# Kernel tuning notes

Hardware: AMD Instinct MI355X
Metric: run time of the kernel (lower is better)

## Reference

```python
import jax, jax.numpy as jnp
import numpy as np
import math

E_LENGTH = 64


def setup_inputs() -> dict:
    key = jax.random.key(0)
    ks = jax.random.split(key, 9)
    B, L, D, N, H = 4, 1024, 1024, 16, 64
    scale = 0.05  # emulate xavier-normal scale
    return {
        "x": jax.random.normal(ks[0], (B, L, D), dtype=jnp.float32),
        "mask": jnp.ones((B, L), dtype=jnp.int32),
        "w_q": jax.random.normal(ks[1], (N, D, H), dtype=jnp.float32) * scale,
        "w_k": jax.random.normal(ks[2], (N, D, H), dtype=jnp.float32) * scale,
        "w_v": jax.random.normal(ks[3], (N, D, H), dtype=jnp.float32) * scale,
        "w_o": jax.random.normal(ks[4], (N, H, D), dtype=jnp.float32) * scale,
        "q_embed_table": jax.random.normal(ks[5], (2 * E_LENGTH - 1, H), dtype=jnp.float32) * scale,
        "k_embed_table": jax.random.normal(ks[6], (2 * E_LENGTH - 1, H), dtype=jnp.float32) * scale,
        "v_embed_table": jax.random.normal(ks[7], (2 * E_LENGTH - 1, H), dtype=jnp.float32) * scale,
    }


def reference(x, mask, w_q, w_k, w_v, w_o, q_embed_table, k_embed_table, v_embed_table):
    # x: [B, L, d_model], mask: [B, L]
    L = x.shape[1]
    d_qkv = w_q.shape[-1]
    e = E_LENGTH

    q = jnp.einsum('blm,nmh->bnlh', x, w_q)
    k = jnp.einsum('blm,nmh->bnlh', x, w_k)
    v = jnp.einsum('blm,nmh->bnlh', x, w_v)

    pos = jnp.arange(L)
    # clipped relative distance indices in [0, 2e-2]
    dist = jnp.clip(pos[:, None] - pos[None, :], -(e - 1), e - 1) + (e - 1)  # [L, L]

    scores = jnp.einsum('bnid,bnjd->bnij', q, k)
    # mode contains 'q': key-side bias uses k_embedding
    k_embed = k_embed_table[dist]  # [L, L, d]
    scores = scores + jnp.einsum('bnjd,ijd->bnij', k, k_embed)
    # mode contains 'k': query-side bias uses q_embedding
    q_embed = q_embed_table[dist]  # [L, L, d]
    scores = scores + jnp.einsum('bnid,ijd->bnij', q, q_embed)

    scores = scores / math.sqrt(d_qkv)
    scores = jnp.where((mask == 0)[:, None, None, :], jnp.float32(-1e9), scores)
    p_attn = jax.nn.softmax(scores, axis=-1)  # [B, N, L, L]

    out = jnp.einsum('bnij,bnjd->bnid', p_attn, v)
    # mode contains 'v': value-side relative bias
    v_embed = v_embed_table[dist]  # [L, L, d]
    out = out + jnp.einsum('bnij,ijd->bnid', p_attn, v_embed)

    # per-head output projection, then sum over heads
    return jnp.einsum('bnid,ndm->bim', out, w_o)
```

## Files before the change

kernel.cpp:

```cpp
#include <hip/hip_runtime.h>


typedef __bf16 bf16x8 __attribute__((ext_vector_type(8)));
typedef float f32x4 __attribute__((ext_vector_type(4)));
typedef unsigned int u32x4 __attribute__((ext_vector_type(4)));
typedef unsigned short u16x4 __attribute__((ext_vector_type(4)));

__device__ __forceinline__ unsigned short f2bf(float f) {
    unsigned int u = __builtin_bit_cast(unsigned int, f);
    u += 0x7fffu + ((u >> 16) & 1u);
    return (unsigned short)(u >> 16);
}
__device__ __forceinline__ float bf2f(unsigned short s) {
    unsigned int u = ((unsigned int)s) << 16;
    return __builtin_bit_cast(float, u);
}

__device__ __forceinline__ void gl2lds16(const unsigned short* g, unsigned short* l) {
    __builtin_amdgcn_global_load_lds(
        (const __attribute__((address_space(1))) unsigned int*)g,
        (__attribute__((address_space(3))) unsigned int*)l, 16, 0, 0);
}

__global__ __launch_bounds__(256) void convert_kernel(
    const float* __restrict__ x,
    const float* __restrict__ wq,
    const float* __restrict__ wk,
    const float* __restrict__ wv,
    const float* __restrict__ wo,
    const float* __restrict__ qe,
    const float* __restrict__ ke,
    const float* __restrict__ ve,
    unsigned short* __restrict__ x_bf,
    unsigned short* __restrict__ wqkv_bt,
    unsigned short* __restrict__ wo_bt,
    unsigned short* __restrict__ qe_bf,
    unsigned short* __restrict__ ke_bf,
    unsigned short* __restrict__ ve_t)
{
    __shared__ unsigned short T[64 * 72];
    const int bid = blockIdx.x;
    const int tid = threadIdx.x;

    if (bid < 512) {
        const float* src = x + (size_t)bid * 8192;
        unsigned short* dst = x_bf + (size_t)bid * 8192;
#pragma unroll
        for (int c = 0; c < 8; ++c) {
            int idx = c * 1024 + tid * 4;
            f32x4 v = *reinterpret_cast<const f32x4*>(src + idx);
            u16x4 o = u16x4{f2bf(v[0]), f2bf(v[1]), f2bf(v[2]), f2bf(v[3])};
            *reinterpret_cast<u16x4*>(dst + idx) = o;
        }
    } else if (bid < 1280) {
        int t = bid - 512;
        int which = t >> 8, n = (t >> 4) & 15, dt = t & 15;
        const float* w = which == 0 ? wq : which == 1 ? wk : wv;
        const float* src = w + ((size_t)n * 1024 + dt * 64) * 64;
#pragma unroll
        for (int c = 0; c < 4; ++c) {
            int chunk = c * 256 + tid;
            int dd = chunk >> 4, hh = (chunk & 15) * 4;
            f32x4 v = *reinterpret_cast<const f32x4*>(src + dd * 64 + hh);
#pragma unroll
            for (int j = 0; j < 4; ++j) T[(hh + j) * 72 + dd] = f2bf(v[j]);
        }
        __syncthreads();
        unsigned short* dstb = wqkv_bt + ((size_t)(which * 1024 + n * 64)) * 1024 + dt * 64;
#pragma unroll
        for (int c = 0; c < 2; ++c) {
            int chunk = c * 256 + tid;
            int h = chunk >> 3, d8 = (chunk & 7) * 8;
            u32x4 v = *reinterpret_cast<const u32x4*>(&T[h * 72 + d8]);
            *reinterpret_cast<u32x4*>(dstb + (size_t)h * 1024 + d8) = v;
        }
    } else if (bid < 1536) {
        int t = bid - 1280;
        int n = t >> 4, mt = t & 15;
        const float* src = wo + (size_t)n * 64 * 1024 + mt * 64;
#pragma unroll
        for (int c = 0; c < 4; ++c) {
            int chunk = c * 256 + tid;
            int hh = chunk >> 4, mm = (chunk & 15) * 4;
            f32x4 v = *reinterpret_cast<const f32x4*>(src + (size_t)hh * 1024 + mm);
#pragma unroll
            for (int j = 0; j < 4; ++j) T[(mm + j) * 72 + hh] = f2bf(v[j]);
        }
        __syncthreads();
        unsigned short* dstb = wo_bt + (size_t)(mt * 64) * 1024 + n * 64;
#pragma unroll
        for (int c = 0; c < 2; ++c) {
            int chunk = c * 256 + tid;
            int m = chunk >> 3, h8 = (chunk & 7) * 8;
            u32x4 v = *reinterpret_cast<const u32x4*>(&T[m * 72 + h8]);
            *reinterpret_cast<u32x4*>(dstb + (size_t)m * 1024 + h8) = v;
        }
    } else {
        for (int i = tid; i < 8192; i += 256) {
            int e = i >> 6;
            qe_bf[i] = (e < 127) ? f2bf(qe[i]) : 0;
            ke_bf[i] = (e < 127) ? f2bf(ke[i]) : 0;
            int h = i >> 7, e2 = i & 127;
            ve_t[i] = (e2 < 127) ? f2bf(ve[e2 * 64 + h]) : 0;
        }
    }
}

__global__ __launch_bounds__(256) void gemm_qkv_kernel(
    const unsigned short* __restrict__ A,
    const unsigned short* __restrict__ Bt,
    unsigned short* __restrict__ q_buf,
    unsigned short* __restrict__ k_buf,
    unsigned short* __restrict__ v_t)
{
    __shared__ unsigned short Sh[2 * 128 * 64];
    unsigned short* As = Sh;
    unsigned short* Bs = Sh + 8192;
    const int m0 = blockIdx.y * 128;
    const int n0 = blockIdx.x * 128;
    const int tid = threadIdx.x;
    const int lane = tid & 63;
    const int w = tid >> 6;
    const int wr = w >> 1, wc = w & 1;
    const int g = lane >> 4, c16 = lane & 15;

    f32x4 acc[4][4];
#pragma unroll
    for (int i = 0; i < 4; ++i)
#pragma unroll
        for (int j = 0; j < 4; ++j) acc[i][j] = f32x4{0.f, 0.f, 0.f, 0.f};

    for (int kt = 0; kt < 1024; kt += 64) {
#pragma unroll
        for (int c = 0; c < 4; ++c) {
            int chunk = c * 256 + tid;
            int row = chunk >> 3, col = (chunk & 7) * 8;
            unsigned short* ldsA = &As[(c * 256 + w * 64) * 8];
            unsigned short* ldsB = &Bs[(c * 256 + w * 64) * 8];
            gl2lds16(A  + (size_t)(m0 + row) * 1024 + kt + col, ldsA);
            gl2lds16(Bt + (size_t)(n0 + row) * 1024 + kt + col, ldsB);
        }
        __syncthreads();
#pragma unroll
        for (int ks = 0; ks < 2; ++ks) {
            bf16x8 af[4], bfr[4];
#pragma unroll
            for (int mi = 0; mi < 4; ++mi)
                af[mi] = __builtin_bit_cast(bf16x8,
                    *reinterpret_cast<const u32x4*>(&As[(wr * 64 + mi * 16 + c16) * 64 + ks * 32 + g * 8]));
#pragma unroll
            for (int ni = 0; ni < 4; ++ni)
                bfr[ni] = __builtin_bit_cast(bf16x8,
                    *reinterpret_cast<const u32x4*>(&Bs[(wc * 64 + ni * 16 + c16) * 64 + ks * 32 + g * 8]));
#pragma unroll
            for (int mi = 0; mi < 4; ++mi)
#pragma unroll
                for (int ni = 0; ni < 4; ++ni)
                    acc[mi][ni] = __builtin_amdgcn_mfma_f32_16x16x32_bf16(af[mi], bfr[ni], acc[mi][ni], 0, 0, 0);
        }
        __syncthreads();
    }

    if (n0 < 2048) {
#pragma unroll
        for (int mi = 0; mi < 4; ++mi)
#pragma unroll
            for (int ni = 0; ni < 4; ++ni)
#pragma unroll
                for (int r = 0; r < 4; ++r) {
                    int m = m0 + wr * 64 + mi * 16 + g * 4 + r;
                    int c = n0 + wc * 64 + ni * 16 + c16;
                    int b = m >> 10, l = m & 1023;
                    int which = c >> 10, n = (c >> 6) & 15, h = c & 63;
                    unsigned short* dst = which == 0 ? q_buf : k_buf;
                    dst[(((size_t)b * 16 + n) * 1024 + l) * 64 + h] = f2bf(acc[mi][ni][r]);
                }
    } else {
#pragma unroll
        for (int mi = 0; mi < 4; ++mi)
#pragma unroll
            for (int ni = 0; ni < 4; ++ni)
#pragma unroll
                for (int r = 0; r < 4; ++r) {
                    int l = wr * 64 + mi * 16 + g * 4 + r;
                    int cr = wc * 64 + ni * 16 + c16;
                    Sh[cr * 128 + (l ^ ((cr & 7) << 3))] = f2bf(acc[mi][ni][r]);
                }
        __syncthreads();
        const int b = m0 >> 10;
        const size_t rowbase = (size_t)(b * 1024 + (n0 - 2048)) * 1024 + (m0 & 1023);
#pragma unroll
        for (int c = 0; c < 8; ++c) {
            int chunk = c * 256 + tid;
            int cr = chunk >> 4, l0 = (chunk & 15) * 8;
            int lsw = l0 ^ ((cr & 7) << 3);
            u32x4 vv = *reinterpret_cast<const u32x4*>(&Sh[cr * 128 + lsw]);
            *reinterpret_cast<u32x4*>(v_t + rowbase + (size_t)cr * 1024 + l0) = vv;
        }
    }
}

__global__ __launch_bounds__(256) void proj_kernel(
    const unsigned short* __restrict__ q_buf,
    const unsigned short* __restrict__ k_buf,
    const unsigned short* __restrict__ qe_bf,
    const unsigned short* __restrict__ ke_bf,
    unsigned short* __restrict__ q_proj,
    unsigned short* __restrict__ k_proj,
    unsigned short* __restrict__ kp_edge)
{
    __shared__ unsigned short As[128 * 64];
    __shared__ unsigned short Bs[128 * 64];
    const int by = blockIdx.y;
    const int which = by >> 9;
    const int m0 = (by & 511) * 128;
    const unsigned short* A  = which ? k_buf : q_buf;
    const unsigned short* Bt = which ? ke_bf : qe_bf;
    unsigned short* C0 = which ? k_proj : q_proj;

    const int tid = threadIdx.x;
    const int lane = tid & 63;
    const int w = tid >> 6;
    const int wr = w >> 1, wc = w & 1;
    const int g = lane >> 4, c16 = lane & 15;

    f32x4 acc[4][4];
#pragma unroll
    for (int i = 0; i < 4; ++i)
#pragma unroll
        for (int j = 0; j < 4; ++j) acc[i][j] = f32x4{0.f, 0.f, 0.f, 0.f};

#pragma unroll
    for (int c = 0; c < 4; ++c) {
        int chunk = c * 256 + tid;
        int row = chunk >> 3, col = (chunk & 7) * 8;
        unsigned short* ldsA = &As[(c * 256 + w * 64) * 8];
        unsigned short* ldsB = &Bs[(c * 256 + w * 64) * 8];
        gl2lds16(A  + (size_t)(m0 + row) * 64 + col, ldsA);
        gl2lds16(Bt + (size_t)row * 64 + col, ldsB);
    }
    __syncthreads();
#pragma unroll
    for (int ks = 0; ks < 2; ++ks) {
        bf16x8 af[4], bfr[4];
#pragma unroll
        for (int mi = 0; mi < 4; ++mi)
            af[mi] = __builtin_bit_cast(bf16x8,
                *reinterpret_cast<const u32x4*>(&As[(wr * 64 + mi * 16 + c16) * 64 + ks * 32 + g * 8]));
#pragma unroll
        for (int ni = 0; ni < 4; ++ni)
            bfr[ni] = __builtin_bit_cast(bf16x8,
                *reinterpret_cast<const u32x4*>(&Bs[(wc * 64 + ni * 16 + c16) * 64 + ks * 32 + g * 8]));
#pragma unroll
        for (int mi = 0; mi < 4; ++mi)
#pragma unroll
            for (int ni = 0; ni < 4; ++ni)
                acc[mi][ni] = __builtin_amdgcn_mfma_f32_16x16x32_bf16(af[mi], bfr[ni], acc[mi][ni], 0, 0, 0);
    }

#pragma unroll
    for (int mi = 0; mi < 4; ++mi) {
#pragma unroll
        for (int ni = 0; ni < 4; ++ni) {
#pragma unroll
            for (int r = 0; r < 4; ++r) {
                int m = m0 + wr * 64 + mi * 16 + g * 4 + r;
                int c = wc * 64 + ni * 16 + c16;
                float v = acc[mi][ni][r];
                C0[(size_t)m * 128 + c] = f2bf(v);
                if (which && (c == 0 || c == 126))
                    kp_edge[(size_t)(c ? 65536 : 0) + m] = f2bf(v);
            }
        }
    }
}

__global__ __launch_bounds__(256) void gemm_n64_kernel(
    const unsigned short* __restrict__ A,
    const unsigned short* __restrict__ Bt,
    float* __restrict__ C)
{
    __shared__ unsigned short As[128 * 64];
    __shared__ unsigned short Bs[64 * 64];
    const int m0 = blockIdx.y * 128;
    const int n0 = blockIdx.x * 64;
    const int tid = threadIdx.x;
    const int lane = tid & 63;
    const int w = tid >> 6;
    const int g = lane >> 4, c16 = lane & 15;

    f32x4 acc[2][4];
#pragma unroll
    for (int i = 0; i < 2; ++i)
#pragma unroll
        for (int j = 0; j < 4; ++j) acc[i][j] = f32x4{0.f, 0.f, 0.f, 0.f};

    for (int kt = 0; kt < 1024; kt += 64) {
#pragma unroll
        for (int c = 0; c < 4; ++c) {
            int chunk = c * 256 + tid;
            int row = chunk >> 3, col = (chunk & 7) * 8;
            unsigned short* ldsA = &As[(c * 256 + w * 64) * 8];
            gl2lds16(A + (size_t)(m0 + row) * 1024 + kt + col, ldsA);
        }
#pragma unroll
        for (int c = 0; c < 2; ++c) {
            int chunk = c * 256 + tid;
            int row = chunk >> 3, col = (chunk & 7) * 8;
            unsigned short* ldsB = &Bs[(c * 256 + w * 64) * 8];
            gl2lds16(Bt + (size_t)(n0 + row) * 1024 + kt + col, ldsB);
        }
        __syncthreads();
#pragma unroll
        for (int ks = 0; ks < 2; ++ks) {
            bf16x8 af[2], bfr[4];
#pragma unroll
            for (int mi = 0; mi < 2; ++mi)
                af[mi] = __builtin_bit_cast(bf16x8,
                    *reinterpret_cast<const u32x4*>(&As[(w * 32 + mi * 16 + c16) * 64 + ks * 32 + g * 8]));
#pragma unroll
            for (int ni = 0; ni < 4; ++ni)
                bfr[ni] = __builtin_bit_cast(bf16x8,
                    *reinterpret_cast<const u32x4*>(&Bs[(ni * 16 + c16) * 64 + ks * 32 + g * 8]));
#pragma unroll
            for (int mi = 0; mi < 2; ++mi)
#pragma unroll
                for (int ni = 0; ni < 4; ++ni)
                    acc[mi][ni] = __builtin_amdgcn_mfma_f32_16x16x32_bf16(af[mi], bfr[ni], acc[mi][ni], 0, 0, 0);
        }
        __syncthreads();
    }

#pragma unroll
    for (int mi = 0; mi < 2; ++mi)
#pragma unroll
        for (int ni = 0; ni < 4; ++ni)
#pragma unroll
            for (int r = 0; r < 4; ++r) {
                int m = m0 + w * 32 + mi * 16 + g * 4 + r;
                int cc = n0 + ni * 16 + c16;
                C[(size_t)m * 1024 + cc] = acc[mi][ni][r];
            }
}

#define ATTN_LDS_BYTES 54784

__global__ __launch_bounds__(512, 4) void attn_kernel(
    const unsigned short* __restrict__ q_buf,
    const unsigned short* __restrict__ k_buf,
    const unsigned short* __restrict__ v_t,
    const unsigned short* __restrict__ q_proj,
    const unsigned short* __restrict__ k_proj,
    const unsigned short* __restrict__ kp_edge,
    const unsigned short* __restrict__ ve_t,
    const int* __restrict__ mask,
    unsigned short* __restrict__ attn_out)
{
    extern __shared__ char smem[];
    unsigned short* Ks = (unsigned short*)smem;
    unsigned short* Vt = (unsigned short*)(smem + 9216);
    unsigned short* Ps = (unsigned short*)(smem + 18432);
    unsigned short* kp = (unsigned short*)(smem + 36864);
    float* mj   = (float*)(smem + 54272);
    float* kpej = (float*)(smem + 54528);
    unsigned short* veT = (unsigned short*)smem;
    unsigned short* peB = (unsigned short*)(smem + 17408);
    float* lrow = (float*)(smem + 52224);

    const int id = blockIdx.x;
    const int bn = id & 63;
    const int ib = id >> 6;
    const int b = bn >> 4;
    const int i0 = ib * 128;
    const int tid = threadIdx.x;
    const int lane = tid & 63;
    const int w = tid >> 6;
    const int g = lane >> 4, c16 = lane & 15;
    const int il = tid >> 2;
    const int part = tid & 3;

    const int jlo = 2 * ib - 1, jhi = 2 * ib + 2;

    const int sr = tid >> 3,  sc = (tid & 7) * 8;

    bf16x8 qf[2];
    {
        const unsigned short* qrow = q_buf + ((size_t)bn * 1024 + i0 + w * 16 + c16) * 64;
        qf[0] = __builtin_bit_cast(bf16x8, *reinterpret_cast<const u32x4*>(qrow + g * 8));
        qf[1] = __builtin_bit_cast(bf16x8, *reinterpret_cast<const u32x4*>(qrow + 32 + g * 8));
    }
    f32x4 qp0v, qp126v;
#pragma unroll
    for (int r = 0; r < 4; ++r) {
        size_t row = (size_t)bn * 1024 + i0 + w * 16 + g * 4 + r;
        qp0v[r]   = 0.125f * bf2f(q_proj[row * 128 + 0]);
        qp126v[r] = 0.125f * bf2f(q_proj[row * 128 + 126]);
    }

    float peR[32];
#pragma unroll
    for (int k = 0; k < 32; ++k) peR[k] = 0.f;
    float lreg = 0.f, acc0 = 0.f, acc126 = 0.f;
    f32x4 accO[4];
#pragma unroll
    for (int i = 0; i < 4; ++i) accO[i] = f32x4{0.f, 0.f, 0.f, 0.f};

    for (int jt = 0; jt < 16; ++jt) {
        const int j0 = jt * 64;
        const bool need_kp = (jt >= jlo) && (jt <= jhi);

        {
            u32x4 kv = *reinterpret_cast<const u32x4*>(k_buf + ((size_t)bn * 1024 + j0 + sr) * 64 + sc);
            u32x4 vv = *reinterpret_cast<const u32x4*>(v_t + ((size_t)bn * 64 + sr) * 1024 + j0 + sc);
            *reinterpret_cast<u32x4*>(&Ks[sr * 72 + sc]) = kv;
            *reinterpret_cast<u32x4*>(&Vt[sr * 72 + sc]) = vv;
        }
        if (need_kp) {
#pragma unroll
            for (int c = 0; c < 2; ++c) {
                int chunk = tid + c * 512;
                int row = chunk >> 4, col = (chunk & 15) * 8;
                u32x4 v = *reinterpret_cast<const u32x4*>(k_proj + ((size_t)bn * 1024 + j0 + row) * 128 + col);
                *reinterpret_cast<u32x4*>(&kp[row * 136 + col]) = v;
            }
        }
        if (tid < 64) {
            mj[tid] = mask[b * 1024 + j0 + tid] ? 1.f : 0.f;
            kpej[tid] = 0.125f * bf2f(kp_edge[(size_t)(jt < 2 * ib ? 65536 : 0) + bn * 1024 + j0 + tid]);
        }
        __syncthreads();

        f32x4 sacc[4];
#pragma unroll
        for (int nf = 0; nf < 4; ++nf) sacc[nf] = f32x4{0.f, 0.f, 0.f, 0.f};
#pragma unroll
        for (int ks = 0; ks < 2; ++ks)
#pragma unroll
            for (int nf = 0; nf < 4; ++nf) {
                bf16x8 kf = __builtin_bit_cast(bf16x8,
                    *reinterpret_cast<const u32x4*>(&Ks[(nf * 16 + c16) * 72 + ks * 32 + g * 8]));
                sacc[nf] = __builtin_amdgcn_mfma_f32_16x16x32_bf16(qf[ks], kf, sacc[nf], 0, 0, 0);
            }

        const int dw = i0 + w * 16 - j0;
        if (dw < 126 && dw > -78) {
            const int d0 = i0 - j0 + 63;
            const unsigned short* qpg = q_proj + ((size_t)bn * 1024 + i0) * 128;
#pragma unroll
            for (int nf = 0; nf < 4; ++nf) {
                int j_l = nf * 16 + c16;
                float mfl = mj[j_l];
#pragma unroll
                for (int r = 0; r < 4; ++r) {
                    int i_l = w * 16 + g * 4 + r;
                    int e = d0 + i_l - j_l;
                    e = e < 0 ? 0 : (e > 126 ? 126 : e);
                    float s = sacc[nf][r] + bf2f(kp[j_l * 136 + e]) + bf2f(qpg[i_l * 128 + e]);
                    s *= 0.125f;
                    float p = (mfl > 0.f) ? __expf(s) : 0.f;
                    Ps[i_l * 72 + j_l] = f2bf(p);
                }
            }
        } else {
            const f32x4 qpc = (dw >= 126) ? qp126v : qp0v;
#pragma unroll
            for (int nf = 0; nf < 4; ++nf) {
                int j_l = nf * 16 + c16;
                float kv = kpej[j_l];
                float mfl = mj[j_l];
#pragma unroll
                for (int r = 0; r < 4; ++r) {
                    float s = sacc[nf][r] * 0.125f + kv + qpc[r];
                    float p = (mfl > 0.f) ? __expf(s) : 0.f;
                    Ps[(w * 16 + g * 4 + r) * 72 + j_l] = f2bf(p);
                }
            }
        }

#pragma unroll
        for (int ks = 0; ks < 2; ++ks) {
            bf16x8 pf = __builtin_bit_cast(bf16x8,
                *reinterpret_cast<const u32x4*>(&Ps[(w * 16 + c16) * 72 + ks * 32 + g * 8]));
#pragma unroll
            for (int nf2 = 0; nf2 < 4; ++nf2) {
                bf16x8 vf = __builtin_bit_cast(bf16x8,
                    *reinterpret_cast<const u32x4*>(&Vt[(nf2 * 16 + c16) * 72 + ks * 32 + g * 8]));
                accO[nf2] = __builtin_amdgcn_mfma_f32_16x16x32_bf16(pf, vf, accO[nf2], 0, 0, 0);
            }
        }

        {
            bf16x8 s0 = __builtin_bit_cast(bf16x8,
                *reinterpret_cast<const u32x4*>(&Ps[il * 72 + part * 16]));
            bf16x8 s1 = __builtin_bit_cast(bf16x8,
                *reinterpret_cast<const u32x4*>(&Ps[il * 72 + part * 16 + 8]));
            float v[16];
#pragma unroll
            for (int m = 0; m < 8; ++m) { v[m] = (float)s0[m]; v[8 + m] = (float)s1[m]; }
            float rs = 0.f;
#pragma unroll
            for (int m = 0; m < 16; ++m) rs += v[m];
            rs += __shfl_xor(rs, 1);
            rs += __shfl_xor(rs, 2);
            lreg += rs;

            const int base = i0 + il - j0 + 63;
            if (base >= 189) {
                acc126 += rs;
            } else if (base <= 0) {
                acc0 += rs;
            } else {
                float b0 = 0.f, b126 = 0.f;
#pragma unroll
                for (int m = 0; m < 16; ++m) {
                    int jl = part * 16 + m;
                    if (jl >= base) b0 += v[m];
                    if (jl <= base - 126) b126 += v[m];
                }
                b0 += __shfl_xor(b0, 1);     b0 += __shfl_xor(b0, 2);
                b126 += __shfl_xor(b126, 1); b126 += __shfl_xor(b126, 2);
                if (part == 0) peR[0] += b0;
                if (part == 3) peR[30] += b126;
#pragma unroll
                for (int k = 0; k < 32; ++k) {
                    int e = part * 32 + k;
                    int jl = base - e;
                    if (e >= 1 && e <= 125 && jl >= 0 && jl < 64)
                        peR[k] += bf2f(Ps[il * 72 + jl]);
                }
            }
        }
        __syncthreads();
    }

    if (part == 0) peR[0] += acc0;
    if (part == 3) peR[30] += acc126;

#pragma unroll
    for (int c = 0; c < 2; ++c) {
        int chunk = tid + c * 512;
        int h = chunk >> 4, col = (chunk & 15) * 8;
        u32x4 vv = *reinterpret_cast<const u32x4*>(ve_t + h * 128 + col);
        *reinterpret_cast<u32x4*>(&veT[h * 136 + col]) = vv;
    }
#pragma unroll
    for (int kk = 0; kk < 4; ++kk) {
        bf16x8 pk;
#pragma unroll
        for (int e2 = 0; e2 < 8; ++e2) pk[e2] = (__bf16)peR[kk * 8 + e2];
        *reinterpret_cast<u32x4*>(&peB[il * 136 + part * 32 + kk * 8]) =
            __builtin_bit_cast(u32x4, pk);
    }
    if (part == 0) lrow[il] = lreg;
    __syncthreads();

#pragma unroll
    for (int ks = 0; ks < 4; ++ks) {
        bf16x8 pf = __builtin_bit_cast(bf16x8,
            *reinterpret_cast<const u32x4*>(&peB[(w * 16 + c16) * 136 + ks * 32 + g * 8]));
#pragma unroll
        for (int nf2 = 0; nf2 < 4; ++nf2) {
            bf16x8 vf = __builtin_bit_cast(bf16x8,
                *reinterpret_cast<const u32x4*>(&veT[(nf2 * 16 + c16) * 136 + ks * 32 + g * 8]));
            accO[nf2] = __builtin_amdgcn_mfma_f32_16x16x32_bf16(pf, vf, accO[nf2], 0, 0, 0);
        }
    }

#pragma unroll
    for (int nf2 = 0; nf2 < 4; ++nf2) {
#pragma unroll
        for (int r = 0; r < 4; ++r) {
            int i_l = w * 16 + g * 4 + r;
            int h = nf2 * 16 + c16;
            float vv = accO[nf2][r] / lrow[i_l];
            attn_out[(((size_t)b * 1024 + i0 + i_l) * 16 + (bn & 15)) * 64 + h] = f2bf(vv);
        }
    }
}

extern "C" void kernel_launch(void* const* d_in, const int* in_sizes, int n_in,
                              void* d_out, int out_size, void* d_ws, size_t ws_size,
                              hipStream_t stream)
{
    const float* x  = (const float*)d_in[0];
    const int* mask = (const int*)d_in[1];
    const float* wq = (const float*)d_in[2];
    const float* wk = (const float*)d_in[3];
    const float* wv = (const float*)d_in[4];
    const float* wo = (const float*)d_in[5];
    const float* qe = (const float*)d_in[6];
    const float* ke = (const float*)d_in[7];
    const float* ve = (const float*)d_in[8];

    char* ws = (char*)d_ws;
    size_t off = 0;
    auto carve = [&](size_t bytes) -> char* {
        char* p = ws + off;
        off += (bytes + 255) & ~(size_t)255;
        return p;
    };
    unsigned short* x_bf    = (unsigned short*)carve(4096ull * 1024 * 2);
    unsigned short* wqkv_bt = (unsigned short*)carve(3072ull * 1024 * 2);
    unsigned short* wo_bt   = (unsigned short*)carve(1024ull * 1024 * 2);
    unsigned short* qe_bf   = (unsigned short*)carve(128ull * 64 * 2);
    unsigned short* ke_bf   = (unsigned short*)carve(128ull * 64 * 2);
    unsigned short* ve_t    = (unsigned short*)carve(64ull * 128 * 2);
    unsigned short* q_buf   = (unsigned short*)carve(65536ull * 64 * 2);
    unsigned short* k_buf   = (unsigned short*)carve(65536ull * 64 * 2);
    unsigned short* v_t     = (unsigned short*)carve(65536ull * 64 * 2);
    unsigned short* q_proj  = (unsigned short*)carve(65536ull * 128 * 2);
    unsigned short* k_proj  = (unsigned short*)carve(65536ull * 128 * 2);
    unsigned short* kp_edge = (unsigned short*)carve(2ull * 65536 * 2);
    unsigned short* attn_o  = x_bf;
    (void)ws_size; (void)in_sizes; (void)n_in; (void)out_size;

    convert_kernel<<<1537, 256, 0, stream>>>(x, wq, wk, wv, wo, qe, ke, ve,
                                             x_bf, wqkv_bt, wo_bt, qe_bf, ke_bf, ve_t);

    gemm_qkv_kernel<<<dim3(24, 32), 256, 0, stream>>>(
        x_bf, wqkv_bt, q_buf, k_buf, v_t);

    proj_kernel<<<dim3(1, 1024), 256, 0, stream>>>(
        q_buf, k_buf, qe_bf, ke_bf, q_proj, k_proj, kp_edge);

    hipFuncSetAttribute((const void*)attn_kernel,
                        hipFuncAttributeMaxDynamicSharedMemorySize, ATTN_LDS_BYTES);
    attn_kernel<<<512, 512, ATTN_LDS_BYTES, stream>>>(
        q_buf, k_buf, v_t, q_proj, k_proj, kp_edge, ve_t, mask, attn_o);

    gemm_n64_kernel<<<dim3(16, 32), 256, 0, stream>>>(attn_o, wo_bt, (float*)d_out);
}
```

Before: 192.8 us.

## Double-buffer K/V tiles with async direct-to-LDS loads and XOR swizzle

K and V^T tiles are now fetched with global_load_lds straight into a double-buffered, XOR-swizzled LDS layout, and the next tile is prefetched while the current one is computed. The mask and edge-bias scalars are staged one tile ahead in the same way. This removes the register round-trip and the per-iteration barrier that sat in front of compute. The k_proj tile also switches to direct-to-LDS loads with unpadded rows, which may cause more bank conflicts, and LDS use per block grows.

Result: faster. 187.9 us, median of 2 (-2.5%).

```diff
diff --git a/kernel.cpp b/kernel.cpp
--- a/kernel.cpp
+++ b/kernel.cpp
@@ -343,7 +343,7 @@
             }
 }
 
-#define ATTN_LDS_BYTES 54784
+#define ATTN_LDS_BYTES 68352
 
 __global__ __launch_bounds__(512, 4) void attn_kernel(
     const unsigned short* __restrict__ q_buf,
@@ -357,12 +357,10 @@
     unsigned short* __restrict__ attn_out)
 {
     extern __shared__ char smem[];
-    unsigned short* Ks = (unsigned short*)smem;
-    unsigned short* Vt = (unsigned short*)(smem + 9216);
-    unsigned short* Ps = (unsigned short*)(smem + 18432);
-    unsigned short* kp = (unsigned short*)(smem + 36864);
-    float* mj   = (float*)(smem + 54272);
-    float* kpej = (float*)(smem + 54528);
+    unsigned short* Ps   = (unsigned short*)(smem + 32768);
+    unsigned short* kp   = (unsigned short*)(smem + 51200);
+    int*            mjI  = (int*)(smem + 67584);
+    unsigned short* kpeU = (unsigned short*)(smem + 68096);
     unsigned short* veT = (unsigned short*)smem;
     unsigned short* peB = (unsigned short*)(smem + 17408);
     float* lrow = (float*)(smem + 52224);
@@ -378,10 +376,39 @@
     const int g = lane >> 4, c16 = lane & 15;
     const int il = tid >> 2;
     const int part = tid & 3;
+    const int swz = c16 & 7;
 
     const int jlo = 2 * ib - 1, jhi = 2 * ib + 2;
 
-    const int sr = tid >> 3,  sc = (tid & 7) * 8;
+    const int srow = w * 8 + (lane >> 3);
+    const int gch  = (lane & 7) ^ (srow & 7);
+
+    auto issue_kv = [&](int j0n, int nxt) {
+        gl2lds16(k_buf + ((size_t)bn * 1024 + j0n + srow) * 64 + gch * 8,
+                 (unsigned short*)(smem + nxt * 8192) + w * 512);
+        gl2lds16(v_t + ((size_t)bn * 64 + srow) * 1024 + j0n + gch * 8,
+                 (unsigned short*)(smem + 16384 + nxt * 8192) + w * 512);
+    };
+    auto stage_scalar = [&](int jtn, int nxt) {
+        int j0n = jtn * 64;
+        if (w == 0) mjI[nxt * 64 + lane] = mask[b * 1024 + j0n + lane];
+        if (w == 1) kpeU[nxt * 64 + lane] =
+            kp_edge[(size_t)(jtn < 2 * ib ? 65536 : 0) + bn * 1024 + j0n + lane];
+    };
+    auto issue_kp = [&](int jtn) {
+        int j0n = jtn * 64;
+#pragma unroll
+        for (int c = 0; c < 2; ++c) {
+            int chunk = w * 128 + c * 64 + lane;
+            int row = chunk >> 4, col8 = chunk & 15;
+            gl2lds16(k_proj + ((size_t)bn * 1024 + j0n + row) * 128 + col8 * 8,
+                     kp + (w * 128 + c * 64) * 8);
+        }
+    };
+
+    issue_kv(0, 0);
+    stage_scalar(0, 0);
+    if (0 >= jlo && 0 <= jhi) issue_kp(0);
 
     bf16x8 qf[2];
     {
@@ -405,30 +432,18 @@
 #pragma unroll
     for (int i = 0; i < 4; ++i) accO[i] = f32x4{0.f, 0.f, 0.f, 0.f};
 
+    __syncthreads();
+
     for (int jt = 0; jt < 16; ++jt) {
+        const int cur = jt & 1;
         const int j0 = jt * 64;
-        const bool need_kp = (jt >= jlo) && (jt <= jhi);
-
-        {
-            u32x4 kv = *reinterpret_cast<const u32x4*>(k_buf + ((size_t)bn * 1024 + j0 + sr) * 64 + sc);
-            u32x4 vv = *reinterpret_cast<const u32x4*>(v_t + ((size_t)bn * 64 + sr) * 1024 + j0 + sc);
-            *reinterpret_cast<u32x4*>(&Ks[sr * 72 + sc]) = kv;
-            *reinterpret_cast<u32x4*>(&Vt[sr * 72 + sc]) = vv;
-        }
-        if (need_kp) {
-#pragma unroll
-            for (int c = 0; c < 2; ++c) {
-                int chunk = tid + c * 512;
-                int row = chunk >> 4, col = (chunk & 15) * 8;
-                u32x4 v = *reinterpret_cast<const u32x4*>(k_proj + ((size_t)bn * 1024 + j0 + row) * 128 + col);
-                *reinterpret_cast<u32x4*>(&kp[row * 136 + col]) = v;
-            }
-        }
-        if (tid < 64) {
-            mj[tid] = mask[b * 1024 + j0 + tid] ? 1.f : 0.f;
-            kpej[tid] = 0.125f * bf2f(kp_edge[(size_t)(jt < 2 * ib ? 65536 : 0) + bn * 1024 + j0 + tid]);
-        }
-        __syncthreads();
+        const unsigned short* Ksc = (const unsigned short*)(smem + cur * 8192);
+        const unsigned short* Vtc = (const unsigned short*)(smem + 16384 + cur * 8192);
+
+        if (jt < 15) {
+            issue_kv(j0 + 64, cur ^ 1);
+            stage_scalar(jt + 1, cur ^ 1);
+        }
 
         f32x4 sacc[4];
 #pragma unroll
@@ -438,7 +453,7 @@
 #pragma unroll
             for (int nf = 0; nf < 4; ++nf) {
                 bf16x8 kf = __builtin_bit_cast(bf16x8,
-                    *reinterpret_cast<const u32x4*>(&Ks[(nf * 16 + c16) * 72 + ks * 32 + g * 8]));
+                    *reinterpret_cast<const u32x4*>(&Ksc[(nf * 16 + c16) * 64 + ((ks * 4 + g) ^ swz) * 8]));
                 sacc[nf] = __builtin_amdgcn_mfma_f32_16x16x32_bf16(qf[ks], kf, sacc[nf], 0, 0, 0);
             }
 
@@ -449,13 +464,13 @@
 #pragma unroll
             for (int nf = 0; nf < 4; ++nf) {
                 int j_l = nf * 16 + c16;
-                float mfl = mj[j_l];
+                float mfl = mjI[cur * 64 + j_l] ? 1.f : 0.f;
 #pragma unroll
                 for (int r = 0; r < 4; ++r) {
                     int i_l = w * 16 + g * 4 + r;
                     int e = d0 + i_l - j_l;
                     e = e < 0 ? 0 : (e > 126 ? 126 : e);
-                    float s = sacc[nf][r] + bf2f(kp[j_l * 136 + e]) + bf2f(qpg[i_l * 128 + e]);
+                    float s = sacc[nf][r] + bf2f(kp[j_l * 128 + e]) + bf2f(qpg[i_l * 128 + e]);
                     s *= 0.125f;
                     float p = (mfl > 0.f) ? __expf(s) : 0.f;
                     Ps[i_l * 72 + j_l] = f2bf(p);
@@ -466,8 +481,8 @@
 #pragma unroll
             for (int nf = 0; nf < 4; ++nf) {
                 int j_l = nf * 16 + c16;
-                float kv = kpej[j_l];
-                float mfl = mj[j_l];
+                float kv = 0.125f * bf2f(kpeU[cur * 64 + j_l]);
+                float mfl = mjI[cur * 64 + j_l] ? 1.f : 0.f;
 #pragma unroll
                 for (int r = 0; r < 4; ++r) {
                     float s = sacc[nf][r] * 0.125f + kv + qpc[r];
@@ -484,7 +499,7 @@
 #pragma unroll
             for (int nf2 = 0; nf2 < 4; ++nf2) {
                 bf16x8 vf = __builtin_bit_cast(bf16x8,
-                    *reinterpret_cast<const u32x4*>(&Vt[(nf2 * 16 + c16) * 72 + ks * 32 + g * 8]));
+                    *reinterpret_cast<const u32x4*>(&Vtc[(nf2 * 16 + c16) * 64 + ((ks * 4 + g) ^ swz) * 8]));
                 accO[nf2] = __builtin_amdgcn_mfma_f32_16x16x32_bf16(pf, vf, accO[nf2], 0, 0, 0);
             }
         }
@@ -530,7 +545,13 @@
                 }
             }
         }
-        __syncthreads();
+
+        const bool kpn = (jt < 15) && (jt + 1 >= jlo) && (jt + 1 <= jhi);
+        __syncthreads();
+        if (kpn) {
+            issue_kp(jt + 1);
+            __syncthreads();
+        }
     }
 
     if (part == 0) peR[0] += acc0;
```
